# Performance work log

Hardware: AMD Instinct MI355X
Metric: run time of the kernel (lower is better)

The kernel has to match this reference:

```python
import jax, jax.numpy as jnp
import numpy as np

HIDDEN = 2048
HEADS = 16
HEAD_DIM = HIDDEN // HEADS
BATCH = 2
SEQ = 2048


def setup_inputs() -> dict:
    key = jax.random.key(0)
    ks = jax.random.split(key, 9)
    s = 0.02
    return {
        "x": jax.random.normal(ks[0], (BATCH, SEQ, HIDDEN), dtype=jnp.float32),
        "Wq": jax.random.normal(ks[1], (HIDDEN, HIDDEN), dtype=jnp.float32) * s,
        "bq": jax.random.normal(ks[2], (HIDDEN,), dtype=jnp.float32) * s,
        "Wk": jax.random.normal(ks[3], (HIDDEN, HIDDEN), dtype=jnp.float32) * s,
        "bk": jax.random.normal(ks[4], (HIDDEN,), dtype=jnp.float32) * s,
        "Wv": jax.random.normal(ks[5], (HIDDEN, HIDDEN), dtype=jnp.float32) * s,
        "bv": jax.random.normal(ks[6], (HIDDEN,), dtype=jnp.float32) * s,
        "Wo": jax.random.normal(ks[7], (HIDDEN, HIDDEN), dtype=jnp.float32) * s,
        "bo": jax.random.normal(ks[8], (HIDDEN,), dtype=jnp.float32) * s,
    }


def reference(x, Wq, bq, Wk, bk, Wv, bv, Wo, bo):
    B, S, H = x.shape
    # Linear layers: y = x @ W.T + b (torch nn.Linear convention, W:[out,in])
    q = x @ Wq.T + bq
    k = x @ Wk.T + bk
    v = x @ Wv.T + bv
    # [B, S, H] -> [B, nH, S, hd]
    def split_heads(t):
        return t.reshape(B, S, HEADS, HEAD_DIM).transpose(0, 2, 1, 3)
    q, k, v = split_heads(q), split_heads(k), split_heads(v)
    scale = 1.0 / (HEAD_DIM ** 0.5)
    # NOTE: original module applies NO causal mask despite its name; be faithful.
    scores = jnp.einsum('bhqd,bhkd->bhqk', q, k) * scale
    probs = jax.nn.softmax(scores, axis=-1)
    attn = jnp.einsum('bhqk,bhkd->bhqd', probs, v)
    attn = attn.transpose(0, 2, 1, 3).reshape(B, S, H)
    return attn @ Wo.T + bo
```

## Files before the change

### kernel.cpp

```cpp
#include <hip/hip_runtime.h>
#include <hip/hip_bf16.h>
#include <stdint.h>

typedef __bf16 bf16_t;
typedef __attribute__((ext_vector_type(8))) __bf16 bf16x8;
typedef __attribute__((ext_vector_type(4))) float floatx4;
typedef __attribute__((ext_vector_type(16))) float f32x16;
typedef __attribute__((ext_vector_type(2))) int i32x2;

typedef __attribute__((address_space(1))) const unsigned int gu32_t;
typedef __attribute__((address_space(3))) unsigned int lu32_t;

__device__ __forceinline__ void async16(const void* g, void* l) {
    __builtin_amdgcn_global_load_lds((gu32_t*)g, (lu32_t*)l, 16, 0, 0);
}

__device__ __forceinline__ uint32_t pack2(float lo, float hi) {
    union { bf16_t h[2]; uint32_t u; } cv;
    cv.h[0] = (bf16_t)lo; cv.h[1] = (bf16_t)hi;
    return cv.u;
}

__global__ __launch_bounds__(256) void cvt_f32_bf16(const float* __restrict__ in,
                                                    bf16_t* __restrict__ out) {
    int i = (blockIdx.x * 256 + threadIdx.x) * 8;
    float4 a = *(const float4*)(in + i);
    float4 b = *(const float4*)(in + i + 4);
    bf16x8 v;
    v[0] = (bf16_t)a.x; v[1] = (bf16_t)a.y; v[2] = (bf16_t)a.z; v[3] = (bf16_t)a.w;
    v[4] = (bf16_t)b.x; v[5] = (bf16_t)b.y; v[6] = (bf16_t)b.z; v[7] = (bf16_t)b.w;
    *(bf16x8*)(out + i) = v;
}

__global__ __launch_bounds__(256) void cvt4_f32_bf16(const float* __restrict__ w0,
                                                     const float* __restrict__ w1,
                                                     const float* __restrict__ w2,
                                                     const float* __restrict__ w3,
                                                     bf16_t* __restrict__ out,
                                                     int elems) {
    const float* srcs[4] = {w0, w1, w2, w3};
    const float* in = srcs[blockIdx.y];
    bf16_t* o = out + (size_t)blockIdx.y * elems;
    int i = (blockIdx.x * 256 + threadIdx.x) * 8;
    float4 a = *(const float4*)(in + i);
    float4 b = *(const float4*)(in + i + 4);
    bf16x8 v;
    v[0] = (bf16_t)a.x; v[1] = (bf16_t)a.y; v[2] = (bf16_t)a.z; v[3] = (bf16_t)a.w;
    v[4] = (bf16_t)b.x; v[5] = (bf16_t)b.y; v[6] = (bf16_t)b.z; v[7] = (bf16_t)b.w;
    *(bf16x8*)(o + i) = v;
}

template <bool OUT_F32, bool BIAS_ROW>
__global__ __launch_bounds__(256) void gemm_bt(const bf16_t* __restrict__ A,
                                               const bf16_t* __restrict__ B,
                                               const float* __restrict__ bias,
                                               const float* __restrict__ bias2,
                                               int nsplit, float scaleA, float scaleB,
                                               float* __restrict__ Cf,
                                               bf16_t* __restrict__ Cb,
                                               int M, int N, int K, int ldc) {
    __shared__ bf16_t As[128 * 64];
    __shared__ bf16_t Bs[128 * 64];
    const int tid = threadIdx.x;
    const int wave = tid >> 6, lane = tid & 63;
    const int quad = lane >> 4, l16 = lane & 15;
    const int wm = (wave >> 1) * 64, wn = (wave & 1) * 64;
    const int tm = blockIdx.x * 128, tn = blockIdx.y * 128;

    floatx4 acc[4][4];
#pragma unroll
    for (int i = 0; i < 4; ++i)
#pragma unroll
        for (int j = 0; j < 4; ++j) acc[i][j] = floatx4{0.f, 0.f, 0.f, 0.f};

    const bf16_t* Abase = A + (size_t)tm * K;
    const bf16_t* Bbase = B + (size_t)tn * K;
    const int sw = l16 & 7;

    for (int kk = 0; kk < K; kk += 64) {
#pragma unroll
        for (int it = 0; it < 4; ++it) {
            int chunk = it * 256 + tid;
            int r = chunk >> 3, c = chunk & 7;
            int c2 = c ^ (r & 7);
            async16(Abase + r * K + kk + c2 * 8, As + (it * 256 + wave * 64) * 8);
            async16(Bbase + r * K + kk + c2 * 8, Bs + (it * 256 + wave * 64) * 8);
        }
        __syncthreads();
#pragma unroll
        for (int ks = 0; ks < 2; ++ks) {
            bf16x8 af[4], bf[4];
#pragma unroll
            for (int mt = 0; mt < 4; ++mt)
                af[mt] = *(const bf16x8*)(As + (wm + mt * 16 + l16) * 64 +
                                          ((ks * 4 + quad) ^ sw) * 8);
#pragma unroll
            for (int nt = 0; nt < 4; ++nt)
                bf[nt] = *(const bf16x8*)(Bs + (wn + nt * 16 + l16) * 64 +
                                          ((ks * 4 + quad) ^ sw) * 8);
#pragma unroll
            for (int mt = 0; mt < 4; ++mt)
#pragma unroll
                for (int nt = 0; nt < 4; ++nt)
                    acc[mt][nt] = __builtin_amdgcn_mfma_f32_16x16x32_bf16(af[mt], bf[nt],
                                                                          acc[mt][nt], 0, 0, 0);
        }
        __syncthreads();
    }
#pragma unroll
    for (int mt = 0; mt < 4; ++mt)
#pragma unroll
        for (int nt = 0; nt < 4; ++nt)
#pragma unroll
            for (int r = 0; r < 4; ++r) {
                int row = tm + wm + mt * 16 + quad * 4 + r;
                int col = tn + wn + nt * 16 + l16;
                float bv = BIAS_ROW ? bias[row]
                                    : (col < nsplit ? bias[col] : bias2[col - nsplit]);
                float v = acc[mt][nt][r] + bv;
                if (!BIAS_ROW) v *= (col < nsplit ? scaleA : scaleB);
                if (OUT_F32) Cf[(size_t)row * ldc + col] = v;
                else Cb[(size_t)row * ldc + col] = (bf16_t)v;
            }
}

template <bool OUT_F32>
__global__ __launch_bounds__(512, 2) void gemm256(const bf16_t* __restrict__ A,
                                                  const bf16_t* __restrict__ B,
                                                  const float* __restrict__ bias,
                                                  const float* __restrict__ bias2,
                                                  int nsplit, float scaleA, float scaleB,
                                                  float* __restrict__ Cf,
                                                  bf16_t* __restrict__ Cb,
                                                  int M, int N, int K, int ldc) {
    __shared__ bf16_t As[2][256 * 64];
    __shared__ bf16_t Bs[2][256 * 64];
    const int tid = threadIdx.x;
    const int wave = tid >> 6, lane = tid & 63;
    const int quad = lane >> 4, l16 = lane & 15;
    const int wr = wave >> 2, wc = wave & 3;
    const int nbx = M >> 8;
    const int nwg = nbx * (N >> 8);
    const int xcd = blockIdx.x & 7, idx = blockIdx.x >> 3;
    const int per = nwg >> 3;
    const int wg = xcd * per + idx;
    const int tm = (wg % nbx) * 256, tn = (wg / nbx) * 256;

    floatx4 acc[8][4];
#pragma unroll
    for (int i = 0; i < 8; ++i)
#pragma unroll
        for (int j = 0; j < 4; ++j) acc[i][j] = floatx4{0.f, 0.f, 0.f, 0.f};

    const bf16_t* Abase = A + (size_t)tm * K;
    const bf16_t* Bbase = B + (size_t)tn * K;
    const int sw2 = (l16 & 4) >> 1;
    const int NT = K >> 6;

    auto stageA = [&](int kk, int b) {
#pragma unroll
        for (int it = 0; it < 4; ++it) {
            int chunk = it * 512 + tid;
            int r = chunk >> 3, c = chunk & 7;
            int c2 = c ^ (((r >> 2) & 1) << 1);
            async16(Abase + (size_t)r * K + kk + c2 * 8, As[b] + chunk * 8);
        }
    };
    auto stageB = [&](int kk, int b) {
#pragma unroll
        for (int it = 0; it < 4; ++it) {
            int chunk = it * 512 + tid;
            int r = chunk >> 3, c = chunk & 7;
            int c2 = c ^ (((r >> 2) & 1) << 1);
            async16(Bbase + (size_t)r * K + kk + c2 * 8, Bs[b] + chunk * 8);
        }
    };

    stageA(0, 0);
    stageB(0, 0);
    asm volatile("s_waitcnt vmcnt(0)" ::: "memory");
    __builtin_amdgcn_s_barrier();
    __builtin_amdgcn_sched_barrier(0);

    for (int t = 0; t < NT; ++t) {
        const int cur = t & 1;
        const bf16_t* Asb = As[cur];
        const bf16_t* Bsb = Bs[cur];
        const int nk = (t + 1) << 6;
        const bool more = (t + 1 < NT);
#pragma unroll
        for (int p = 0; p < 4; ++p) {
            const int mh = p >> 1, nh = p & 1;
            bf16x8 af[4][2], bg[2][2];
#pragma unroll
            for (int mt = 0; mt < 4; ++mt) {
                int row = wr * 128 + mh * 64 + mt * 16 + l16;
#pragma unroll
                for (int ks = 0; ks < 2; ++ks)
                    af[mt][ks] = *(const bf16x8*)(Asb + row * 64 + ((ks * 4 + quad) ^ sw2) * 8);
            }
#pragma unroll
            for (int nt = 0; nt < 2; ++nt) {
                int col = wc * 64 + nh * 32 + nt * 16 + l16;
#pragma unroll
                for (int ks = 0; ks < 2; ++ks)
                    bg[nt][ks] = *(const bf16x8*)(Bsb + col * 64 + ((ks * 4 + quad) ^ sw2) * 8);
            }
            if (more) {
                if (p == 0) stageA(nk, cur ^ 1);
                else if (p == 1) stageB(nk, cur ^ 1);
            }
            __builtin_amdgcn_s_barrier();
            asm volatile("s_waitcnt lgkmcnt(0)" ::: "memory");
            __builtin_amdgcn_sched_barrier(0);
            __builtin_amdgcn_s_setprio(1);
#pragma unroll
            for (int ks = 0; ks < 2; ++ks)
#pragma unroll
                for (int mt = 0; mt < 4; ++mt)
#pragma unroll
                    for (int nt = 0; nt < 2; ++nt)
                        acc[mh * 4 + mt][nh * 2 + nt] =
                            __builtin_amdgcn_mfma_f32_16x16x32_bf16(
                                af[mt][ks], bg[nt][ks], acc[mh * 4 + mt][nh * 2 + nt], 0, 0, 0);
            __builtin_amdgcn_s_setprio(0);
            if (p == 3 && more)
                asm volatile("s_waitcnt vmcnt(0)" ::: "memory");
            __builtin_amdgcn_s_barrier();
            __builtin_amdgcn_sched_barrier(0);
        }
    }

#pragma unroll
    for (int am = 0; am < 8; ++am)
#pragma unroll
        for (int an = 0; an < 4; ++an)
#pragma unroll
            for (int r = 0; r < 4; ++r) {
                int row = tm + wr * 128 + (am >> 2) * 64 + (am & 3) * 16 + quad * 4 + r;
                int col = tn + wc * 64 + (an >> 1) * 32 + (an & 1) * 16 + l16;
                float bv = col < nsplit ? bias[col] : bias2[col - nsplit];
                float v = (acc[am][an][r] + bv) * (col < nsplit ? scaleA : scaleB);
                if (OUT_F32) Cf[(size_t)row * ldc + col] = v;
                else Cb[(size_t)row * ldc + col] = (bf16_t)v;
            }
}

#define KELEMS (64 * 128)
#define VELEMS (128 * 64)
__global__ __launch_bounds__(256, 2) void flash_attn(const bf16_t* __restrict__ Qp,
                                                     const bf16_t* __restrict__ Kp,
                                                     const bf16_t* __restrict__ Vt,
                                                     bf16_t* __restrict__ O) {
    __shared__ bf16_t smem[2 * KELEMS + 2 * VELEMS];
    const int tid = threadIdx.x;
    const int wv = tid >> 6, lane = tid & 63;
    const int hi = lane >> 5, l32 = lane & 31;
    const int wq = wv >> 1, wk = wv & 1;
    const int LD = 4096, T = 4096, S = 2048, HO = 2048;

    const int gid = blockIdx.x;
    const int kq = gid >> 3;
    const int qt = kq & 31;
    const int grp = (gid & 7) + 8 * (kq >> 5);
    const int hd = grp & 15, bt = grp >> 4;

    const int qrow0 = bt * S + qt * 64;
    const int krow0 = bt * S;
    const int hoff = hd * 128;
    const int sw7 = l32 & 7;
    const int swK = l32 & 15;

    bf16x8 qf[8];
    const bf16_t* qptr = Qp + (size_t)(qrow0 + wq * 32 + l32) * LD + hoff + hi * 8;
#pragma unroll
    for (int ks = 0; ks < 8; ++ks) qf[ks] = *(const bf16x8*)(qptr + ks * 16);

    float l_i = 0.f;
    f32x16 Oacc[4];
#pragma unroll
    for (int dt = 0; dt < 4; ++dt)
#pragma unroll
        for (int r = 0; r < 16; ++r) Oacc[dt][r] = 0.f;

    auto stageK = [&](int kt, int b) {
        int kb = krow0 + kt * 64;
        bf16_t* Ks = smem + b * KELEMS;
#pragma unroll
        for (int it = 0; it < 4; ++it) {
            int chunk = it * 256 + tid;
            int r = chunk >> 4, c = chunk & 15;
            int c2 = c ^ (r & 15);
            async16(Kp + (size_t)(kb + r) * LD + hoff + c2 * 8, Ks + chunk * 8);
        }
    };
    auto stageV = [&](int kt, int b) {
        int kb = krow0 + kt * 64;
        bf16_t* Vts = smem + 2 * KELEMS + b * VELEMS;
#pragma unroll
        for (int it = 0; it < 4; ++it) {
            int chunk = it * 256 + tid;
            int r = chunk >> 3, c = chunk & 7;
            int c2 = c ^ (r & 7);
            async16(Vt + (size_t)(hoff + r) * T + kb + c2 * 8, Vts + chunk * 8);
        }
    };

    auto pv = [&](const uint32_t* pk, int vb) {
        const bf16_t* Vts = smem + 2 * KELEMS + vb * VELEMS;
#pragma unroll
        for (int s = 0; s < 2; ++s) {
            i32x2 s02 = __builtin_amdgcn_permlane32_swap((int)pk[4 * s + 0],
                                                         (int)pk[4 * s + 2], false, false);
            i32x2 s13 = __builtin_amdgcn_permlane32_swap((int)pk[4 * s + 1],
                                                         (int)pk[4 * s + 3], false, false);
            union { uint32_t u[4]; bf16x8 v; } w;
            w.u[0] = (uint32_t)s02[0];
            w.u[1] = (uint32_t)s13[0];
            w.u[2] = (uint32_t)s02[1];
            w.u[3] = (uint32_t)s13[1];
#pragma unroll
            for (int dt = 0; dt < 4; ++dt) {
                bf16x8 a = *(const bf16x8*)(Vts + (dt * 32 + l32) * 64 +
                                            ((4 * wk + 2 * s + hi) ^ sw7) * 8);
                Oacc[dt] = __builtin_amdgcn_mfma_f32_32x32x16_bf16(a, w.v, Oacc[dt], 0, 0, 0);
            }
        }
    };

    uint32_t pkPrev[8];
    stageK(0, 0);
    stageV(0, 0);
    for (int kt = 0; kt < 32; ++kt) {
        const int cur = kt & 1;
        __syncthreads();
        if (kt + 1 < 32) stageK(kt + 1, cur ^ 1);

        const bf16_t* Ks = smem + cur * KELEMS;

        f32x16 sf0, sf1;
#pragma unroll
        for (int r = 0; r < 16; ++r) { sf0[r] = 0.f; sf1[r] = 0.f; }
#pragma unroll
        for (int ks = 0; ks < 4; ++ks) {
            bf16x8 a0 = *(const bf16x8*)(Ks + (wk * 32 + l32) * 128 +
                                         ((2 * ks + hi) ^ swK) * 8);
            bf16x8 a1 = *(const bf16x8*)(Ks + (wk * 32 + l32) * 128 +
                                         ((2 * (ks + 4) + hi) ^ swK) * 8);
            sf0 = __builtin_amdgcn_mfma_f32_32x32x16_bf16(a0, qf[ks], sf0, 0, 0, 0);
            sf1 = __builtin_amdgcn_mfma_f32_32x32x16_bf16(a1, qf[ks + 4], sf1, 0, 0, 0);
        }

        if (kt > 0) pv(pkPrev, cur ^ 1);

        __syncthreads();
        if (kt + 1 < 32) stageV(kt + 1, cur ^ 1);

        float rs0 = 0.f, rs1 = 0.f;
#pragma unroll
        for (int a4 = 0; a4 < 4; ++a4) {
            float p0 = exp2f(sf0[4 * a4 + 0] + sf1[4 * a4 + 0]);
            float p1 = exp2f(sf0[4 * a4 + 1] + sf1[4 * a4 + 1]);
            float p2 = exp2f(sf0[4 * a4 + 2] + sf1[4 * a4 + 2]);
            float p3 = exp2f(sf0[4 * a4 + 3] + sf1[4 * a4 + 3]);
            rs0 += p0 + p1;
            rs1 += p2 + p3;
            pkPrev[a4 * 2 + 0] = pack2(p0, p1);
            pkPrev[a4 * 2 + 1] = pack2(p2, p3);
        }
        l_i += rs0 + rs1;
    }

    pv(pkPrev, 1);

    __syncthreads();
    l_i += __shfl_xor(l_i, 32);
    float* ml = (float*)smem;
    if (hi == 0) ml[wv * 32 + l32] = l_i;
    __syncthreads();
    float linv = 1.0f / (l_i + ml[(wv ^ 1) * 32 + l32]);
    __syncthreads();

    float* Op = (float*)smem;
    if (wk == 1) {
#pragma unroll
        for (int dt = 0; dt < 4; ++dt)
#pragma unroll
            for (int r = 0; r < 16; ++r) {
                int d = dt * 32 + (r & 3) + 8 * (r >> 2) + 4 * hi;
                Op[(wq * 128 + d) * 32 + l32] = Oacc[dt][r];
            }
    }
    __syncthreads();
    if (wk == 0) {
#pragma unroll
        for (int dt = 0; dt < 4; ++dt)
#pragma unroll
            for (int r = 0; r < 16; ++r) {
                int d = dt * 32 + (r & 3) + 8 * (r >> 2) + 4 * hi;
                Oacc[dt][r] = (Oacc[dt][r] + Op[(wq * 128 + d) * 32 + l32]) * linv;
            }
    }
    __syncthreads();

    if (wk == 0) {
        uint32_t* Os = (uint32_t*)smem + wq * 2048;
#pragma unroll
        for (int dt = 0; dt < 4; ++dt)
#pragma unroll
            for (int a4 = 0; a4 < 4; ++a4) {
                uint32_t q0 = pack2(Oacc[dt][4 * a4 + 0], Oacc[dt][4 * a4 + 1]);
                uint32_t q1 = pack2(Oacc[dt][4 * a4 + 2], Oacc[dt][4 * a4 + 3]);
                int d2 = 16 * dt + 4 * a4 + 2 * hi;
                Os[l32 * 64 + ((d2 + 2 * l32) & 63)] = q0;
                Os[l32 * 64 + ((d2 + 1 + 2 * l32) & 63)] = q1;
            }
#pragma unroll
        for (int r = 0; r < 32; ++r) {
            uint32_t v = Os[r * 64 + ((lane + 2 * r) & 63)];
            uint32_t* orow = (uint32_t*)(O + (size_t)(qrow0 + wq * 32 + r) * HO + hoff);
            orow[lane] = v;
        }
    }
}

extern "C" void kernel_launch(void* const* d_in, const int* in_sizes, int n_in,
                              void* d_out, int out_size, void* d_ws, size_t ws_size,
                              hipStream_t stream) {
    const float* x  = (const float*)d_in[0];
    const float* Wq = (const float*)d_in[1];
    const float* bq = (const float*)d_in[2];
    const float* Wk = (const float*)d_in[3];
    const float* bk = (const float*)d_in[4];
    const float* Wv = (const float*)d_in[5];
    const float* bv = (const float*)d_in[6];
    const float* Wo = (const float*)d_in[7];
    const float* bo = (const float*)d_in[8];
    float* out = (float*)d_out;

    const int T = 4096;
    const int H = 2048;
    const float SL2E = 0.088388347688f * 1.44269504089f;
    bf16_t* ws  = (bf16_t*)d_ws;
    bf16_t* xb  = ws;
    bf16_t* wqb = xb  + (size_t)T * H;
    bf16_t* wkb = wqb + (size_t)H * H;
    bf16_t* wvb = wkb + (size_t)H * H;
    bf16_t* wob = wvb + (size_t)H * H;
    bf16_t* QKb = wob + (size_t)H * H;
    bf16_t* Vtb = QKb + (size_t)T * 2 * H;
    bf16_t* Ab  = Vtb + (size_t)H * T;
    size_t need = (size_t)(Ab + (size_t)T * H - ws) * sizeof(bf16_t);
    if (ws_size < need) return;

    cvt_f32_bf16<<<T * H / 2048, 256, 0, stream>>>(x, xb);
    cvt4_f32_bf16<<<dim3(H * H / 2048, 4), 256, 0, stream>>>(Wq, Wk, Wv, Wo, wqb, H * H);

    gemm256<false><<<(T / 256) * (4096 / 256), 512, 0, stream>>>(
        xb, wqb, bq, bk, H, SL2E, 1.0f, nullptr, QKb, T, 4096, H, 4096);

    dim3 gv(H / 128, T / 128);
    gemm_bt<false, true><<<gv, 256, 0, stream>>>(wvb, xb, bv, nullptr, 0, 1.0f, 1.0f,
                                                 nullptr, Vtb, H, T, H, T);

    flash_attn<<<1024, 256, 0, stream>>>(QKb, QKb + H, Vtb, Ab);

    dim3 go(T / 128, H / 128);
    gemm_bt<true, false><<<go, 256, 0, stream>>>(Ab, wob, bo, nullptr, H, 1.0f, 1.0f,
                                                 out, nullptr, T, H, H, H);
}
```

Measured before the change: 411.6 us.

## Double-buffer GEMM register fragments, widen LDS swizzle, merge conversion kernels

Inside the 256x256 QK projection GEMM, the LDS fragment loads for the next phase are now issued before the current phase's MFMAs, using two alternating register fragment sets, so LDS reads overlap with matrix math. The LDS XOR swizzle changes from a 1-bit pattern to a full 3-bit row-based XOR, applied the same way on the write and read sides, to reduce bank conflicts. The two f32-to-bf16 conversion launches are merged into a single launch that covers both x and the four weight matrices. The extra fragment buffers raise register pressure, which could lower occupancy or cause spills.

```diff
diff --git a/kernel.cpp b/kernel.cpp
--- a/kernel.cpp
+++ b/kernel.cpp
@@ -21,33 +21,33 @@
     return cv.u;
 }
 
-__global__ __launch_bounds__(256) void cvt_f32_bf16(const float* __restrict__ in,
-                                                    bf16_t* __restrict__ out) {
-    int i = (blockIdx.x * 256 + threadIdx.x) * 8;
+__global__ __launch_bounds__(256) void cvt_all(const float* __restrict__ x,
+                                               const float* __restrict__ w0,
+                                               const float* __restrict__ w1,
+                                               const float* __restrict__ w2,
+                                               const float* __restrict__ w3,
+                                               bf16_t* __restrict__ xb,
+                                               bf16_t* __restrict__ wb) {
+    const int b = blockIdx.x;
+    const float* in;
+    bf16_t* out;
+    int local;
+    if (b < 4096) {
+        in = x; out = xb; local = b;
+    } else {
+        int wi = (b - 4096) >> 11;
+        const float* srcs[4] = {w0, w1, w2, w3};
+        in = srcs[wi];
+        out = wb + (size_t)wi * 2048 * 2048;
+        local = (b - 4096) & 2047;
+    }
+    int i = (local * 256 + threadIdx.x) * 8;
     float4 a = *(const float4*)(in + i);
-    float4 b = *(const float4*)(in + i + 4);
+    float4 c = *(const float4*)(in + i + 4);
     bf16x8 v;
     v[0] = (bf16_t)a.x; v[1] = (bf16_t)a.y; v[2] = (bf16_t)a.z; v[3] = (bf16_t)a.w;
-    v[4] = (bf16_t)b.x; v[5] = (bf16_t)b.y; v[6] = (bf16_t)b.z; v[7] = (bf16_t)b.w;
+    v[4] = (bf16_t)c.x; v[5] = (bf16_t)c.y; v[6] = (bf16_t)c.z; v[7] = (bf16_t)c.w;
     *(bf16x8*)(out + i) = v;
-}
-
-__global__ __launch_bounds__(256) void cvt4_f32_bf16(const float* __restrict__ w0,
-                                                     const float* __restrict__ w1,
-                                                     const float* __restrict__ w2,
-                                                     const float* __restrict__ w3,
-                                                     bf16_t* __restrict__ out,
-                                                     int elems) {
-    const float* srcs[4] = {w0, w1, w2, w3};
-    const float* in = srcs[blockIdx.y];
-    bf16_t* o = out + (size_t)blockIdx.y * elems;
-    int i = (blockIdx.x * 256 + threadIdx.x) * 8;
-    float4 a = *(const float4*)(in + i);
-    float4 b = *(const float4*)(in + i + 4);
-    bf16x8 v;
-    v[0] = (bf16_t)a.x; v[1] = (bf16_t)a.y; v[2] = (bf16_t)a.z; v[3] = (bf16_t)a.w;
-    v[4] = (bf16_t)b.x; v[5] = (bf16_t)b.y; v[6] = (bf16_t)b.z; v[7] = (bf16_t)b.w;
-    *(bf16x8*)(o + i) = v;
 }
 
 template <bool OUT_F32, bool BIAS_ROW>
@@ -154,7 +154,7 @@
 
     const bf16_t* Abase = A + (size_t)tm * K;
     const bf16_t* Bbase = B + (size_t)tn * K;
-    const int sw2 = (l16 & 4) >> 1;
+    const int sw = l16 & 7;
     const int NT = K >> 6;
 
     auto stageA = [&](int kk, int b) {
@@ -162,7 +162,7 @@
         for (int it = 0; it < 4; ++it) {
             int chunk = it * 512 + tid;
             int r = chunk >> 3, c = chunk & 7;
-            int c2 = c ^ (((r >> 2) & 1) << 1);
+            int c2 = c ^ (r & 7);
             async16(Abase + (size_t)r * K + kk + c2 * 8, As[b] + chunk * 8);
         }
     };
@@ -171,7 +171,7 @@
         for (int it = 0; it < 4; ++it) {
             int chunk = it * 512 + tid;
             int r = chunk >> 3, c = chunk & 7;
-            int c2 = c ^ (((r >> 2) & 1) << 1);
+            int c2 = c ^ (r & 7);
             async16(Bbase + (size_t)r * K + kk + c2 * 8, Bs[b] + chunk * 8);
         }
     };
@@ -188,24 +188,41 @@
         const bf16_t* Bsb = Bs[cur];
         const int nk = (t + 1) << 6;
         const bool more = (t + 1 < NT);
-#pragma unroll
-        for (int p = 0; p < 4; ++p) {
-            const int mh = p >> 1, nh = p & 1;
-            bf16x8 af[4][2], bg[2][2];
+
+        auto ldq = [&](int ph, bf16x8 (&af)[4][2], bf16x8 (&bg)[2][2]) {
+            const int mh = ph >> 1, nh = ph & 1;
 #pragma unroll
             for (int mt = 0; mt < 4; ++mt) {
                 int row = wr * 128 + mh * 64 + mt * 16 + l16;
 #pragma unroll
                 for (int ks = 0; ks < 2; ++ks)
-                    af[mt][ks] = *(const bf16x8*)(Asb + row * 64 + ((ks * 4 + quad) ^ sw2) * 8);
+                    af[mt][ks] = *(const bf16x8*)(Asb + row * 64 + ((ks * 4 + quad) ^ sw) * 8);
             }
 #pragma unroll
             for (int nt = 0; nt < 2; ++nt) {
                 int col = wc * 64 + nh * 32 + nt * 16 + l16;
 #pragma unroll
                 for (int ks = 0; ks < 2; ++ks)
-                    bg[nt][ks] = *(const bf16x8*)(Bsb + col * 64 + ((ks * 4 + quad) ^ sw2) * 8);
-            }
+                    bg[nt][ks] = *(const bf16x8*)(Bsb + col * 64 + ((ks * 4 + quad) ^ sw) * 8);
+            }
+        };
+        auto domfma = [&](int ph, bf16x8 (&af)[4][2], bf16x8 (&bg)[2][2]) {
+            const int mh = ph >> 1, nh = ph & 1;
+#pragma unroll
+            for (int ks = 0; ks < 2; ++ks)
+#pragma unroll
+                for (int mt = 0; mt < 4; ++mt)
+#pragma unroll
+                    for (int nt = 0; nt < 2; ++nt)
+                        acc[mh * 4 + mt][nh * 2 + nt] =
+                            __builtin_amdgcn_mfma_f32_16x16x32_bf16(
+                                af[mt][ks], bg[nt][ks], acc[mh * 4 + mt][nh * 2 + nt], 0, 0, 0);
+        };
+
+        bf16x8 afA[4][2], bgA[2][2], afB[4][2], bgB[2][2];
+        ldq(0, afA, bgA);
+#pragma unroll
+        for (int p = 0; p < 4; ++p) {
             if (more) {
                 if (p == 0) stageA(nk, cur ^ 1);
                 else if (p == 1) stageB(nk, cur ^ 1);
@@ -214,15 +231,13 @@
             asm volatile("s_waitcnt lgkmcnt(0)" ::: "memory");
             __builtin_amdgcn_sched_barrier(0);
             __builtin_amdgcn_s_setprio(1);
-#pragma unroll
-            for (int ks = 0; ks < 2; ++ks)
-#pragma unroll
-                for (int mt = 0; mt < 4; ++mt)
-#pragma unroll
-                    for (int nt = 0; nt < 2; ++nt)
-                        acc[mh * 4 + mt][nh * 2 + nt] =
-                            __builtin_amdgcn_mfma_f32_16x16x32_bf16(
-                                af[mt][ks], bg[nt][ks], acc[mh * 4 + mt][nh * 2 + nt], 0, 0, 0);
+            if ((p & 1) == 0) {
+                if (p < 3) ldq(p + 1, afB, bgB);
+                domfma(p, afA, bgA);
+            } else {
+                if (p < 3) ldq(p + 1, afA, bgA);
+                domfma(p, afB, bgB);
+            }
             __builtin_amdgcn_s_setprio(0);
             if (p == 3 && more)
                 asm volatile("s_waitcnt vmcnt(0)" ::: "memory");
@@ -453,8 +468,7 @@
     size_t need = (size_t)(Ab + (size_t)T * H - ws) * sizeof(bf16_t);
     if (ws_size < need) return;
 
-    cvt_f32_bf16<<<T * H / 2048, 256, 0, stream>>>(x, xb);
-    cvt4_f32_bf16<<<dim3(H * H / 2048, 4), 256, 0, stream>>>(Wq, Wk, Wv, Wo, wqb, H * H);
+    cvt_all<<<12288, 256, 0, stream>>>(x, Wq, Wk, Wv, Wo, xb, wqb);
 
     gemm256<false><<<(T / 256) * (4096 / 256), 512, 0, stream>>>(
         xb, wqb, bq, bk, H, SL2E, 1.0f, nullptr, QKb, T, 4096, H, 4096);
```

Measured after the change: 402.9 us. 2.1% less time.
